# Kernel tuning notes

Measured on AMD Instinct MI355X. Metric: run time of the kernel, lower is better.

The kernel has to match this reference:

```python
import jax, jax.numpy as jnp
import numpy as np

N, S, D, H = 2, 2048, 1024, 16
DH = D // H  # 64


def setup_inputs() -> dict:
    key = jax.random.key(0)
    ks = jax.random.split(key, 7)
    scale = 1.0 / np.sqrt(DH)  # ~nn.Linear default init range
    return {
        "sequences": jax.random.normal(ks[0], (N, S, D), dtype=jnp.float32),
        "Wq": jax.random.uniform(ks[1], (H, DH, DH), jnp.float32, -scale, scale),
        "bq": jax.random.uniform(ks[2], (H, DH), jnp.float32, -scale, scale),
        "Wk": jax.random.uniform(ks[3], (H, DH, DH), jnp.float32, -scale, scale),
        "bk": jax.random.uniform(ks[4], (H, DH), jnp.float32, -scale, scale),
        "Wv": jax.random.uniform(ks[5], (H, DH, DH), jnp.float32, -scale, scale),
        "bv": jax.random.uniform(ks[6], (H, DH), jnp.float32, -scale, scale),
    }


def reference(sequences, Wq, bq, Wk, bk, Wv, bv):
    n, s, d = sequences.shape
    x = sequences.reshape(n, s, H, DH)  # [N,S,H,Dh]
    # per-head Linear: y = x @ W^T + b, batched over heads
    q = jnp.einsum('nshd,hed->nshe', x, Wq) + bq  # [N,S,H,Dh]
    k = jnp.einsum('nshd,hed->nshe', x, Wk) + bk
    v = jnp.einsum('nshd,hed->nshe', x, Wv) + bv
    # attention: scores [N,H,S,S]
    scores = jnp.einsum('nqhd,nkhd->nhqk', q, k) / jnp.sqrt(jnp.float32(DH))
    w = jax.nn.softmax(scores, axis=-1)
    out = jnp.einsum('nhqk,nkhd->nqhd', w, v)  # [N,S,H,Dh]
    return out.reshape(n, s, d)
```

## Files before the change

kernel.cpp:

```cpp
#include <hip/hip_runtime.h>
#include <hip/hip_bf16.h>


#define NB 2
#define SS 2048
#define DM 1024
#define NH 16
#define DHd 64

typedef __attribute__((ext_vector_type(8))) short bf16x8;
typedef __attribute__((ext_vector_type(4))) float f32x4;

union U8 { bf16x8 v; unsigned short u[8]; };

__device__ __forceinline__ unsigned short f2b(float x) {
    __hip_bfloat16 h = __float2bfloat16(x);
    return *reinterpret_cast<unsigned short*>(&h);
}

__device__ __forceinline__ bf16x8 pack8(float4 a, float4 b) {
    U8 t;
    t.u[0] = f2b(a.x); t.u[1] = f2b(a.y); t.u[2] = f2b(a.z); t.u[3] = f2b(a.w);
    t.u[4] = f2b(b.x); t.u[5] = f2b(b.y); t.u[6] = f2b(b.z); t.u[7] = f2b(b.w);
    return t.v;
}

__device__ __forceinline__ int swz(int row, int ch) {
    return row * 64 + ((ch ^ (row & 7)) * 8);
}

#define QSCALE 0.18033688011112042f

__global__ __launch_bounds__(256) void qkv_proj(
    const float* __restrict__ seq,
    const float* __restrict__ Wq, const float* __restrict__ bq,
    const float* __restrict__ Wk, const float* __restrict__ bk,
    const float* __restrict__ Wv, const float* __restrict__ bv,
    unsigned short* __restrict__ Q, unsigned short* __restrict__ K,
    unsigned short* __restrict__ Vt)
{
    __shared__ unsigned short Xl[128 * 64];
    __shared__ unsigned short Wl[3 * 64 * 64];

    const int tid = threadIdx.x;
    const int wv = tid >> 6, L = tid & 63, lo = L & 15, qd = L >> 4;
    const int bi = blockIdx.x;
    const int nh = bi >> 4, sb = bi & 15;
    const int h = nh & (NH - 1), n = nh >> 4;
    const int s0 = sb * 128;

#pragma unroll
    for (int i = 0; i < 4; ++i) {
        int idx = tid + i * 256;
        int r = idx >> 3, ch = idx & 7;
        const float* src = seq + ((size_t)(n * SS + s0 + r)) * DM + h * DHd + ch * 8;
        float4 a = ((const float4*)src)[0];
        float4 b = ((const float4*)src)[1];
        *(bf16x8*)&Xl[swz(r, ch)] = pack8(a, b);
    }
#pragma unroll
    for (int i = 0; i < 6; ++i) {
        int idx = tid + i * 256;
        int mat = idx >> 9;
        int rem = idx & 511;
        int e = rem >> 3, ch = rem & 7;
        const float* Wm = (mat == 0) ? Wq : (mat == 1) ? Wk : Wv;
        const float* src = Wm + (size_t)(h * DHd + e) * DHd + ch * 8;
        float4 a = ((const float4*)src)[0];
        float4 b = ((const float4*)src)[1];
        *(bf16x8*)&Wl[mat * 4096 + swz(e, ch)] = pack8(a, b);
    }
    __syncthreads();

    bf16x8 xf[2][2];
#pragma unroll
    for (int st = 0; st < 2; ++st)
#pragma unroll
        for (int kt = 0; kt < 2; ++kt)
            xf[st][kt] = *(const bf16x8*)&Xl[swz(wv * 32 + st * 16 + lo, kt * 4 + qd)];

#pragma unroll
    for (int m2 = 0; m2 < 2; ++m2) {
        const unsigned short* Wb = &Wl[m2 * 4096];
        const float* bias = m2 ? bk : bq;
        unsigned short* O = m2 ? K : Q;
        const float sc = m2 ? 1.0f : QSCALE;

        f32x4 acc[4][2];
#pragma unroll
        for (int et = 0; et < 4; ++et) {
            float4 bb = *(const float4*)&bias[h * DHd + et * 16 + qd * 4];
#pragma unroll
            for (int st = 0; st < 2; ++st)
                acc[et][st] = (f32x4){bb.x, bb.y, bb.z, bb.w};
        }
#pragma unroll
        for (int et = 0; et < 4; ++et) {
            bf16x8 wf0 = *(const bf16x8*)&Wb[swz(et * 16 + lo, qd)];
            bf16x8 wf1 = *(const bf16x8*)&Wb[swz(et * 16 + lo, 4 + qd)];
#pragma unroll
            for (int st = 0; st < 2; ++st) {
                acc[et][st] = __builtin_amdgcn_mfma_f32_16x16x32_bf16(
                    wf0, xf[st][0], acc[et][st], 0, 0, 0);
                acc[et][st] = __builtin_amdgcn_mfma_f32_16x16x32_bf16(
                    wf1, xf[st][1], acc[et][st], 0, 0, 0);
            }
        }
#pragma unroll
        for (int et = 0; et < 4; ++et)
#pragma unroll
            for (int st = 0; st < 2; ++st) {
                int s = s0 + wv * 32 + st * 16 + lo;
                ushort4 w;
                w.x = f2b(acc[et][st][0] * sc); w.y = f2b(acc[et][st][1] * sc);
                w.z = f2b(acc[et][st][2] * sc); w.w = f2b(acc[et][st][3] * sc);
                *(ushort4*)&O[((size_t)nh * SS + s) * DHd + et * 16 + qd * 4] = w;
            }
    }

    {
        const unsigned short* Wb = &Wl[2 * 4096];
        float bvv[4];
#pragma unroll
        for (int et = 0; et < 4; ++et) bvv[et] = bv[h * DHd + et * 16 + lo];

        f32x4 acc[2][4];
#pragma unroll
        for (int st = 0; st < 2; ++st)
#pragma unroll
            for (int et = 0; et < 4; ++et)
                acc[st][et] = (f32x4){bvv[et], bvv[et], bvv[et], bvv[et]};
#pragma unroll
        for (int et = 0; et < 4; ++et) {
            bf16x8 wf0 = *(const bf16x8*)&Wb[swz(et * 16 + lo, qd)];
            bf16x8 wf1 = *(const bf16x8*)&Wb[swz(et * 16 + lo, 4 + qd)];
#pragma unroll
            for (int st = 0; st < 2; ++st) {
                acc[st][et] = __builtin_amdgcn_mfma_f32_16x16x32_bf16(
                    xf[st][0], wf0, acc[st][et], 0, 0, 0);
                acc[st][et] = __builtin_amdgcn_mfma_f32_16x16x32_bf16(
                    xf[st][1], wf1, acc[st][et], 0, 0, 0);
            }
        }
#pragma unroll
        for (int st = 0; st < 2; ++st)
#pragma unroll
            for (int et = 0; et < 4; ++et) {
                int e = et * 16 + lo;
                int s = s0 + wv * 32 + st * 16 + qd * 4;
                ushort4 w;
                w.x = f2b(acc[st][et][0]); w.y = f2b(acc[st][et][1]);
                w.z = f2b(acc[st][et][2]); w.w = f2b(acc[st][et][3]);
                *(ushort4*)&Vt[((size_t)nh * DHd + e) * SS + s] = w;
            }
    }
}

#define PSTR 72
#define THR 3.0f

__global__ __launch_bounds__(256) void attn(
    const unsigned short* __restrict__ Qg, const unsigned short* __restrict__ Kg,
    const unsigned short* __restrict__ Vg, float* __restrict__ out)
{
    __shared__ unsigned short Kl[64 * 64];
    __shared__ unsigned short Vl[64 * 64];
    __shared__ unsigned short Pl[4][32 * PSTR];

    const int tid = threadIdx.x;
    const int wv = tid >> 6, L = tid & 63, lo = L & 15, qd = L >> 4;
    const int bi = blockIdx.x;
    const int nh = bi >> 4, qblk = bi & 15;
    const int h = nh & (NH - 1), n = nh >> 4;
    const int q0 = qblk * 128 + wv * 32;

    const unsigned short* Qnh = Qg + (size_t)nh * SS * DHd;
    const unsigned short* Knh = Kg + (size_t)nh * SS * DHd;
    const unsigned short* Vnh = Vg + (size_t)nh * DHd * SS;

    const int r0 = tid >> 3, c0 = tid & 7;

    bf16x8 qf[2][2];
#pragma unroll
    for (int ct = 0; ct < 2; ++ct)
#pragma unroll
        for (int kt = 0; kt < 2; ++kt)
            qf[ct][kt] = *(const bf16x8*)(Qnh + (size_t)(q0 + ct * 16 + lo) * DHd
                                          + kt * 32 + qd * 8);

    f32x4 oacc[4][2];
#pragma unroll
    for (int rt = 0; rt < 4; ++rt)
#pragma unroll
        for (int ct = 0; ct < 2; ++ct)
            oacc[rt][ct] = (f32x4){0.f, 0.f, 0.f, 0.f};

    float m[2] = {-1e30f, -1e30f};
    float l[2] = {0.f, 0.f};

    uint4 ks0 = *(const uint4*)(Knh + (size_t)r0 * DHd + c0 * 8);
    uint4 ks1 = *(const uint4*)(Knh + (size_t)(r0 + 32) * DHd + c0 * 8);
    uint4 vs0 = *(const uint4*)(Vnh + (size_t)r0 * SS + c0 * 8);
    uint4 vs1 = *(const uint4*)(Vnh + (size_t)(r0 + 32) * SS + c0 * 8);

    for (int t = 0; t < SS / 64; ++t) {
        __syncthreads();
        *(uint4*)&Kl[swz(r0, c0)]      = ks0;
        *(uint4*)&Kl[swz(r0 + 32, c0)] = ks1;
        *(uint4*)&Vl[swz(r0, c0)]      = vs0;
        *(uint4*)&Vl[swz(r0 + 32, c0)] = vs1;
        __syncthreads();

        if (t + 1 < SS / 64) {
            const int kn = (t + 1) * 64;
            ks0 = *(const uint4*)(Knh + (size_t)(kn + r0) * DHd + c0 * 8);
            ks1 = *(const uint4*)(Knh + (size_t)(kn + r0 + 32) * DHd + c0 * 8);
            vs0 = *(const uint4*)(Vnh + (size_t)r0 * SS + kn + c0 * 8);
            vs1 = *(const uint4*)(Vnh + (size_t)(r0 + 32) * SS + kn + c0 * 8);
        }

        f32x4 sacc[4][2];
#pragma unroll
        for (int rt = 0; rt < 4; ++rt)
#pragma unroll
            for (int ct = 0; ct < 2; ++ct)
                sacc[rt][ct] = (f32x4){0.f, 0.f, 0.f, 0.f};
        __builtin_amdgcn_s_setprio(1);
#pragma unroll
        for (int rt = 0; rt < 4; ++rt)
#pragma unroll
            for (int kt = 0; kt < 2; ++kt) {
                bf16x8 kf = *(const bf16x8*)&Kl[swz(rt * 16 + lo, kt * 4 + qd)];
#pragma unroll
                for (int ct = 0; ct < 2; ++ct)
                    sacc[rt][ct] = __builtin_amdgcn_mfma_f32_16x16x32_bf16(
                        kf, qf[ct][kt], sacc[rt][ct], 0, 0, 0);
            }
        __builtin_amdgcn_s_setprio(0);

#pragma unroll
        for (int ct = 0; ct < 2; ++ct) {
            float mx = sacc[0][ct][0];
#pragma unroll
            for (int rt = 0; rt < 4; ++rt)
#pragma unroll
                for (int r = 0; r < 4; ++r)
                    mx = fmaxf(mx, sacc[rt][ct][r]);
            mx = fmaxf(mx, __shfl_xor(mx, 16, 64));
            mx = fmaxf(mx, __shfl_xor(mx, 32, 64));
            if (__any(mx > m[ct] + THR)) {
                const float mn = fmaxf(m[ct], mx);
                const float corr = __builtin_amdgcn_exp2f(m[ct] - mn);
                l[ct] *= corr;
#pragma unroll
                for (int rt = 0; rt < 4; ++rt)
#pragma unroll
                    for (int r = 0; r < 4; ++r)
                        oacc[rt][ct][r] *= corr;
                m[ct] = mn;
            }
            const float mb = m[ct];
            float rs = 0.f;
#pragma unroll
            for (int rt = 0; rt < 4; ++rt) {
                float p0 = __builtin_amdgcn_exp2f(sacc[rt][ct][0] - mb);
                float p1 = __builtin_amdgcn_exp2f(sacc[rt][ct][1] - mb);
                float p2 = __builtin_amdgcn_exp2f(sacc[rt][ct][2] - mb);
                float p3 = __builtin_amdgcn_exp2f(sacc[rt][ct][3] - mb);
                rs += (p0 + p1) + (p2 + p3);
                ushort4 w;
                w.x = f2b(p0); w.y = f2b(p1); w.z = f2b(p2); w.w = f2b(p3);
                *(ushort4*)&Pl[wv][(ct * 16 + lo) * PSTR + rt * 16 + qd * 4] = w;
            }
            l[ct] += rs;
        }

        __builtin_amdgcn_s_setprio(1);
#pragma unroll
        for (int kt = 0; kt < 2; ++kt) {
            bf16x8 pf[2];
#pragma unroll
            for (int ct = 0; ct < 2; ++ct)
                pf[ct] = *(const bf16x8*)&Pl[wv][(ct * 16 + lo) * PSTR
                                                 + kt * 32 + qd * 8];
#pragma unroll
            for (int rt = 0; rt < 4; ++rt) {
                bf16x8 vf = *(const bf16x8*)&Vl[swz(rt * 16 + lo, kt * 4 + qd)];
#pragma unroll
                for (int ct = 0; ct < 2; ++ct)
                    oacc[rt][ct] = __builtin_amdgcn_mfma_f32_16x16x32_bf16(
                        vf, pf[ct], oacc[rt][ct], 0, 0, 0);
            }
        }
        __builtin_amdgcn_s_setprio(0);
    }

#pragma unroll
    for (int ct = 0; ct < 2; ++ct) {
        float lt = l[ct];
        lt += __shfl_xor(lt, 16, 64);
        lt += __shfl_xor(lt, 32, 64);
        const float inv = 1.0f / lt;
        const int s = q0 + ct * 16 + lo;
#pragma unroll
        for (int rt = 0; rt < 4; ++rt) {
            float4 o;
            o.x = oacc[rt][ct][0] * inv; o.y = oacc[rt][ct][1] * inv;
            o.z = oacc[rt][ct][2] * inv; o.w = oacc[rt][ct][3] * inv;
            *(float4*)&out[((size_t)n * SS + s) * DM + h * DHd
                           + rt * 16 + qd * 4] = o;
        }
    }
}

extern "C" void kernel_launch(void* const* d_in, const int* in_sizes, int n_in,
                              void* d_out, int out_size, void* d_ws, size_t ws_size,
                              hipStream_t stream) {
    const float* seq = (const float*)d_in[0];
    const float* Wq  = (const float*)d_in[1];
    const float* bq  = (const float*)d_in[2];
    const float* Wk  = (const float*)d_in[3];
    const float* bk  = (const float*)d_in[4];
    const float* Wv  = (const float*)d_in[5];
    const float* bv  = (const float*)d_in[6];
    float* out = (float*)d_out;

    const size_t per = (size_t)NB * NH * SS * DHd;
    unsigned short* Q  = (unsigned short*)d_ws;
    unsigned short* K  = Q + per;
    unsigned short* Vt = K + per;

    qkv_proj<<<512, 256, 0, stream>>>(seq, Wq, bq, Wk, bk, Wv, bv, Q, K, Vt);
    attn<<<512, 256, 0, stream>>>(Q, K, Vt, out);
}
```

Baseline: 144.9 us.

## Double-buffer K/V shared tiles to drop one barrier per iteration

K and V shared-memory tiles become double-buffered. The next tile is written into the alternate buffer after the PV MMAs, and global loads are issued two tiles ahead. This removes one of the two __syncthreads per loop iteration and gives the register-staged global loads a full iteration of latency to hide. In exchange, LDS use for K/V doubles (from 16KB to 32KB), which may reduce occupancy, and register pressure stays the same.

Result: no change. 143.8 us (-0.8%).

```diff
diff --git a/kernel.cpp b/kernel.cpp
--- a/kernel.cpp
+++ b/kernel.cpp
@@ -158,13 +158,14 @@
 
 #define PSTR 72
 #define THR 3.0f
+#define NT (SS / 64)
 
 __global__ __launch_bounds__(256) void attn(
     const unsigned short* __restrict__ Qg, const unsigned short* __restrict__ Kg,
     const unsigned short* __restrict__ Vg, float* __restrict__ out)
 {
-    __shared__ unsigned short Kl[64 * 64];
-    __shared__ unsigned short Vl[64 * 64];
+    __shared__ unsigned short Kl[2][64 * 64];
+    __shared__ unsigned short Vl[2][64 * 64];
     __shared__ unsigned short Pl[4][32 * PSTR];
 
     const int tid = threadIdx.x;
@@ -202,22 +203,18 @@
     uint4 ks1 = *(const uint4*)(Knh + (size_t)(r0 + 32) * DHd + c0 * 8);
     uint4 vs0 = *(const uint4*)(Vnh + (size_t)r0 * SS + c0 * 8);
     uint4 vs1 = *(const uint4*)(Vnh + (size_t)(r0 + 32) * SS + c0 * 8);
-
-    for (int t = 0; t < SS / 64; ++t) {
-        __syncthreads();
-        *(uint4*)&Kl[swz(r0, c0)]      = ks0;
-        *(uint4*)&Kl[swz(r0 + 32, c0)] = ks1;
-        *(uint4*)&Vl[swz(r0, c0)]      = vs0;
-        *(uint4*)&Vl[swz(r0 + 32, c0)] = vs1;
-        __syncthreads();
-
-        if (t + 1 < SS / 64) {
-            const int kn = (t + 1) * 64;
-            ks0 = *(const uint4*)(Knh + (size_t)(kn + r0) * DHd + c0 * 8);
-            ks1 = *(const uint4*)(Knh + (size_t)(kn + r0 + 32) * DHd + c0 * 8);
-            vs0 = *(const uint4*)(Vnh + (size_t)r0 * SS + kn + c0 * 8);
-            vs1 = *(const uint4*)(Vnh + (size_t)(r0 + 32) * SS + kn + c0 * 8);
-        }
+    *(uint4*)&Kl[0][swz(r0, c0)]      = ks0;
+    *(uint4*)&Kl[0][swz(r0 + 32, c0)] = ks1;
+    *(uint4*)&Vl[0][swz(r0, c0)]      = vs0;
+    *(uint4*)&Vl[0][swz(r0 + 32, c0)] = vs1;
+    ks0 = *(const uint4*)(Knh + (size_t)(64 + r0) * DHd + c0 * 8);
+    ks1 = *(const uint4*)(Knh + (size_t)(64 + r0 + 32) * DHd + c0 * 8);
+    vs0 = *(const uint4*)(Vnh + (size_t)r0 * SS + 64 + c0 * 8);
+    vs1 = *(const uint4*)(Vnh + (size_t)(r0 + 32) * SS + 64 + c0 * 8);
+    __syncthreads();
+
+    for (int t = 0; t < NT; ++t) {
+        const int cur = t & 1;
 
         f32x4 sacc[4][2];
 #pragma unroll
@@ -230,7 +227,7 @@
         for (int rt = 0; rt < 4; ++rt)
 #pragma unroll
             for (int kt = 0; kt < 2; ++kt) {
-                bf16x8 kf = *(const bf16x8*)&Kl[swz(rt * 16 + lo, kt * 4 + qd)];
+                bf16x8 kf = *(const bf16x8*)&Kl[cur][swz(rt * 16 + lo, kt * 4 + qd)];
 #pragma unroll
                 for (int ct = 0; ct < 2; ++ct)
                     sacc[rt][ct] = __builtin_amdgcn_mfma_f32_16x16x32_bf16(
@@ -278,21 +275,36 @@
         __builtin_amdgcn_s_setprio(1);
 #pragma unroll
         for (int kt = 0; kt < 2; ++kt) {
-            bf16x8 pf[2];
+            bf16x8 pfr[2];
 #pragma unroll
             for (int ct = 0; ct < 2; ++ct)
-                pf[ct] = *(const bf16x8*)&Pl[wv][(ct * 16 + lo) * PSTR
-                                                 + kt * 32 + qd * 8];
+                pfr[ct] = *(const bf16x8*)&Pl[wv][(ct * 16 + lo) * PSTR
+                                                  + kt * 32 + qd * 8];
 #pragma unroll
             for (int rt = 0; rt < 4; ++rt) {
-                bf16x8 vf = *(const bf16x8*)&Vl[swz(rt * 16 + lo, kt * 4 + qd)];
+                bf16x8 vf = *(const bf16x8*)&Vl[cur][swz(rt * 16 + lo, kt * 4 + qd)];
 #pragma unroll
                 for (int ct = 0; ct < 2; ++ct)
                     oacc[rt][ct] = __builtin_amdgcn_mfma_f32_16x16x32_bf16(
-                        vf, pf[ct], oacc[rt][ct], 0, 0, 0);
+                        vf, pfr[ct], oacc[rt][ct], 0, 0, 0);
             }
         }
         __builtin_amdgcn_s_setprio(0);
+
+        if (t + 1 < NT) {
+            *(uint4*)&Kl[cur ^ 1][swz(r0, c0)]      = ks0;
+            *(uint4*)&Kl[cur ^ 1][swz(r0 + 32, c0)] = ks1;
+            *(uint4*)&Vl[cur ^ 1][swz(r0, c0)]      = vs0;
+            *(uint4*)&Vl[cur ^ 1][swz(r0 + 32, c0)] = vs1;
+            if (t + 2 < NT) {
+                const int kn = (t + 2) * 64;
+                ks0 = *(const uint4*)(Knh + (size_t)(kn + r0) * DHd + c0 * 8);
+                ks1 = *(const uint4*)(Knh + (size_t)(kn + r0 + 32) * DHd + c0 * 8);
+                vs0 = *(const uint4*)(Vnh + (size_t)r0 * SS + kn + c0 * 8);
+                vs1 = *(const uint4*)(Vnh + (size_t)(r0 + 32) * SS + kn + c0 * 8);
+            }
+        }
+        __syncthreads();
     }
 
 #pragma unroll
```
